# Optimization experiments

Hardware: AMD Instinct MI355X
Metric: run time of the kernel (lower is better)

## Reference

```python
import jax, jax.numpy as jnp
import numpy as np

B, N_NODES, NUM_FEATURES = 64, 1024, 128
NHID = 128
NUM_CLASSES = 10
SKEW_DIM = 64
EDGES_PER_GRAPH = 16384
POOL_RATIO = 0.5
LAMB = 1.0
NEG_SLOPE = 0.2  # HGPSLPool default negative_slope


def setup_inputs() -> dict:
    key = jax.random.key(0)
    ks = jax.random.split(key, 16)
    x = jax.random.normal(ks[0], (B, N_NODES, NUM_FEATURES), jnp.float32)
    src = jax.random.randint(ks[1], (B, EDGES_PER_GRAPH), 0, N_NODES)
    dst = jax.random.randint(ks[2], (B, EDGES_PER_GRAPH), 0, N_NODES)
    skew = jax.random.normal(ks[3], (B, SKEW_DIM), jnp.float32)

    def glorot(k, shape):
        s = jnp.sqrt(6.0 / (shape[0] + shape[1]))
        return jax.random.uniform(k, shape, jnp.float32, -s, s)

    params = dict(
        W1=glorot(ks[4], (NUM_FEATURES, NHID)), b1=jnp.zeros((NHID,), jnp.float32),
        W2=glorot(ks[5], (NHID, NHID)), b2=jnp.zeros((NHID,), jnp.float32),
        W3=glorot(ks[6], (NHID, NHID)), b3=jnp.zeros((NHID,), jnp.float32),
        att1=glorot(ks[7], (2 * NHID, 1))[:, 0],
        att2=glorot(ks[8], (2 * NHID, 1))[:, 0],
        Wsk=glorot(ks[9], (SKEW_DIM, NHID)), bsk=jnp.zeros((NHID,), jnp.float32),
        Wl1=glorot(ks[10], (3 * NHID, NHID)), bl1=jnp.zeros((NHID,), jnp.float32),
        Wl2=glorot(ks[11], (NHID, NHID // 2)), bl2=jnp.zeros((NHID // 2,), jnp.float32),
        Wl3=glorot(ks[12], (NHID // 2, NUM_CLASSES)), bl3=jnp.zeros((NUM_CLASSES,), jnp.float32),
    )
    return {"x": x, "src": src, "dst": dst, "skew": skew, **params}


def _inv_sqrt(d):
    return jnp.where(d > 0, jax.lax.rsqrt(jnp.where(d > 0, d, 1.0)), 0.0)


def gcn_conv(X, A, W, b):
    # x' = D^-1/2 (A + I_missing) D^-1/2 (X W) + b  (add_remaining_self_loops fill=1)
    n = A.shape[-1]
    diag = jnp.diagonal(A, axis1=-2, axis2=-1)  # [B,n]
    A_sl = A + jnp.where(diag == 0, 1.0, 0.0)[:, :, None] * jnp.eye(n, dtype=A.dtype)
    dis = _inv_sqrt(A_sl.sum(-1))  # [B,n]
    h = X @ W
    return dis[:, :, None] * jnp.einsum('bij,bjf->bif', A_sl, dis[:, :, None] * h) + b


def node_information_score(X, A):
    # (I - D^-1/2 A D^-1/2) X with self-loops removed; score = row-sum of |.|
    A0 = A * (1.0 - jnp.eye(A.shape[-1], dtype=A.dtype))
    dis = _inv_sqrt(A0.sum(-1))
    Anorm = dis[:, :, None] * A0 * dis[:, None, :]
    info = X - jnp.einsum('bij,bjf->bif', Anorm, X)
    return jnp.abs(info).sum(-1)  # [B,n]


def hgpsl_pool(X, A, att, k):
    # top-k by information score, induced subgraph, dense structure learning (softmax attn)
    score = node_information_score(X, A)
    _, perm = jax.lax.top_k(score, k)  # [B,k]
    Xp = jnp.take_along_axis(X, perm[:, :, None], axis=1)  # [B,k,F]
    Ap = jnp.take_along_axis(jnp.take_along_axis(A, perm[:, :, None], axis=1), perm[:, None, :], axis=2)
    F_ = X.shape[-1]
    a_row = Xp @ att[:F_]  # [B,k]
    a_col = Xp @ att[F_:]
    w = jax.nn.leaky_relu(a_row[:, :, None] + a_col[:, None, :], NEG_SLOPE)
    w = w + LAMB * Ap  # induced edge weights (ones on binary graph) scaled by lamb
    A_new = jax.nn.softmax(w, axis=-1)  # per-row softmax over within-graph nodes
    return Xp, A_new


def readout(X):
    return jnp.concatenate([X.max(axis=1), X.mean(axis=1)], axis=-1)  # [gmp | gap]


def reference(x, src, dst, skew, W1, b1, W2, b2, W3, b3, att1, att2, Wsk, bsk,
              Wl1, bl1, Wl2, bl2, Wl3, bl3):
    Bn, n = x.shape[0], x.shape[1]
    b_idx = jnp.arange(Bn)[:, None]
    A = jnp.zeros((Bn, n, n), x.dtype).at[b_idx, src, dst].set(1.0)
    A = jnp.maximum(A, A.transpose(0, 2, 1)) * (1.0 - jnp.eye(n, dtype=x.dtype))

    xskew = jax.nn.relu(skew @ Wsk + bsk)  # [B, nhid]

    h = jax.nn.relu(gcn_conv(x, A, W1, b1))
    k1 = int(np.ceil(POOL_RATIO * n))
    h, A1 = hgpsl_pool(h, A, att1, k1)
    x1 = readout(h)

    h = jax.nn.relu(gcn_conv(h, A1, W2, b2))
    k2 = int(np.ceil(POOL_RATIO * k1))
    h, A2 = hgpsl_pool(h, A1, att2, k2)
    x2 = readout(h)

    h = jax.nn.relu(gcn_conv(h, A2, W3, b3))
    x3 = readout(h)

    g = jax.nn.relu(x1) + jax.nn.relu(x2) + jax.nn.relu(x3)  # [B, 2*nhid]
    g = jnp.concatenate([g, xskew], axis=-1)                  # [B, 3*nhid]
    g = jax.nn.relu(g @ Wl1 + bl1)  # dropout is identity in eval mode
    g = jax.nn.relu(g @ Wl2 + bl2)
    return jax.nn.log_softmax(g @ Wl3 + bl3, axis=-1)
```

## Files before the change

### kernel.cpp

```cpp
#include <hip/hip_runtime.h>
#include <math.h>

#define Bb 64
#define N0 1024
#define NE 16384
#define Fd 128
#define K1 512
#define K2 256
#define RPB 256

typedef __attribute__((ext_vector_type(8))) short short8v;
typedef __attribute__((ext_vector_type(4))) float float4v;

__device__ __forceinline__ float wred_sum(float v) {
#pragma unroll
  for (int o = 32; o > 0; o >>= 1) v += __shfl_down(v, o, 64);
  return v;
}
__device__ __forceinline__ float wred_sum_all(float v) {
#pragma unroll
  for (int o = 32; o > 0; o >>= 1) v += __shfl_xor(v, o, 64);
  return v;
}
__device__ __forceinline__ float wred_max_all(float v) {
#pragma unroll
  for (int o = 32; o > 0; o >>= 1) v = fmaxf(v, __shfl_xor(v, o, 64));
  return v;
}
__device__ __forceinline__ unsigned short bf16hi(float x) {
  unsigned u = __float_as_uint(x);
  return (unsigned short)((u + 0x7fffu + ((u >> 16) & 1u)) >> 16);
}
__device__ __forceinline__ float bf2f(unsigned short h) {
  return __uint_as_float(((unsigned)h) << 16);
}

__global__ __launch_bounds__(1024) void k_graph(const int* __restrict__ src,
    const int* __restrict__ dst, unsigned* __restrict__ adj,
    unsigned short* __restrict__ nbr, int* __restrict__ degv,
    float* __restrict__ dis0, float* __restrict__ dis1) {
  __shared__ unsigned lmask[RPB * 32];
  int t = threadIdx.x;
  int b = blockIdx.x >> 2;
  int rlo = (blockIdx.x & 3) * RPB;
#pragma unroll
  for (int i = t; i < RPB * 32; i += 1024) lmask[i] = 0;
  __syncthreads();
  const int* sp = src + b * NE;
  const int* dp = dst + b * NE;
#pragma unroll
  for (int e = t; e < NE; e += 1024) {
    int u = sp[e], v = dp[e];
    if (u == v) continue;
    if ((unsigned)(u - rlo) < RPB)
      atomicOr(&lmask[(u - rlo) * 32 + (v >> 5)], 1u << (v & 31));
    if ((unsigned)(v - rlo) < RPB)
      atomicOr(&lmask[(v - rlo) * 32 + (u >> 5)], 1u << (u & 31));
  }
  __syncthreads();
  unsigned* adjg = adj + ((size_t)(b << 10) + rlo) * 32;
#pragma unroll
  for (int i = t; i < RPB * 32; i += 1024) adjg[i] = lmask[i];
  if (t < RPB) {
    int row = (b << 10) + rlo + t;
    const unsigned* wm = &lmask[t * 32];
    int d = 0;
#pragma unroll
    for (int i = 0; i < 32; ++i) d += __popc(wm[i]);
    degv[row] = d;
    dis0[row] = d > 0 ? rsqrtf((float)d) : 0.f;
    dis1[row] = rsqrtf((float)(d + 1));
    unsigned short* dstp = nbr + (size_t)row * 128;
    int o = 0;
#pragma unroll
    for (int w = 0; w < 32; ++w) {
      unsigned m = wm[w];
      int bas = w << 5;
      while (m) {
        int j = bas + __ffs(m) - 1; m &= m - 1;
        dstp[o++] = (unsigned short)((j << 2) | (j & 3));
      }
    }
  }
}

__global__ __launch_bounds__(512) void k_gemmm(const float* __restrict__ X,
                                               const float* __restrict__ W,
                                               float* __restrict__ C) {
  __shared__ unsigned short AsHi[64 * 40], AsLo[64 * 40];
  __shared__ unsigned short YtHi[128 * 40], YtLo[128 * 40];
  int t = threadIdx.x;
  size_t row0 = (size_t)blockIdx.x * 64;
  const float* Xb = X + row0 * Fd;
  int sar = t >> 3, sak = (t & 7) << 2;
  int awoff = sar * 40 + ((sak >> 3) ^ ((sar >> 3) & 3)) * 8 + (sak & 4);
  int wc = t & 127, ob = t >> 7;
  int ywoff = wc * 40 + (ob ^ ((wc >> 3) & 3)) * 8;
  int w = t >> 6, l = t & 63;
  int tr = w & 3, ch = w >> 2;
  int lr = l & 15, lg4 = l >> 4;
  int arow = 16 * tr + lr;
  int aroff = arow * 40 + ((lg4 ^ ((arow >> 3) & 3)) << 3);
  int boff[4];
#pragma unroll
  for (int j = 0; j < 4; ++j) {
    int colj = ch * 64 + j * 16 + lr;
    boff[j] = colj * 40 + ((lg4 ^ ((colj >> 3) & 3)) << 3);
  }
  float4v acc[4] = {{0.f, 0.f, 0.f, 0.f}, {0.f, 0.f, 0.f, 0.f},
                    {0.f, 0.f, 0.f, 0.f}, {0.f, 0.f, 0.f, 0.f}};
  for (int kb = 0; kb < 128; kb += 32) {
    __syncthreads();
    {
      float4 av = *(const float4*)&Xb[(size_t)sar * Fd + kb + sak];
      float vs[4] = {av.x, av.y, av.z, av.w};
      unsigned short h[4], lo[4];
#pragma unroll
      for (int i = 0; i < 4; ++i) {
        h[i] = bf16hi(vs[i]);
        float fhi = __uint_as_float(((unsigned)h[i]) << 16);
        lo[i] = bf16hi(vs[i] - fhi);
      }
      uint2 ph, pl;
      ph.x = (unsigned)h[0] | ((unsigned)h[1] << 16);
      ph.y = (unsigned)h[2] | ((unsigned)h[3] << 16);
      pl.x = (unsigned)lo[0] | ((unsigned)lo[1] << 16);
      pl.y = (unsigned)lo[2] | ((unsigned)lo[3] << 16);
      *(uint2*)&AsHi[awoff] = ph;
      *(uint2*)&AsLo[awoff] = pl;
    }
    {
      float vs[8];
      const float* wp = W + (size_t)(kb + ob * 8) * Fd + wc;
#pragma unroll
      for (int kk = 0; kk < 8; ++kk) vs[kk] = wp[(size_t)kk * Fd];
      uint4 uh, ul;
      unsigned hu[4], lu[4];
#pragma unroll
      for (int kk = 0; kk < 4; ++kk) {
        unsigned short h0 = bf16hi(vs[2 * kk]);
        unsigned short l0 = bf16hi(vs[2 * kk] - __uint_as_float(((unsigned)h0) << 16));
        unsigned short h1 = bf16hi(vs[2 * kk + 1]);
        unsigned short l1 = bf16hi(vs[2 * kk + 1] - __uint_as_float(((unsigned)h1) << 16));
        hu[kk] = (unsigned)h0 | ((unsigned)h1 << 16);
        lu[kk] = (unsigned)l0 | ((unsigned)l1 << 16);
      }
      uh.x = hu[0]; uh.y = hu[1]; uh.z = hu[2]; uh.w = hu[3];
      ul.x = lu[0]; ul.y = lu[1]; ul.z = lu[2]; ul.w = lu[3];
      *(uint4*)&YtHi[ywoff] = uh;
      *(uint4*)&YtLo[ywoff] = ul;
    }
    __syncthreads();
    short8v ah = *(const short8v*)&AsHi[aroff];
    short8v al = *(const short8v*)&AsLo[aroff];
#pragma unroll
    for (int j = 0; j < 4; ++j) {
      short8v bh = *(const short8v*)&YtHi[boff[j]];
      short8v bl = *(const short8v*)&YtLo[boff[j]];
      acc[j] = __builtin_amdgcn_mfma_f32_16x16x32_bf16(ah, bh, acc[j], 0, 0, 0);
      acc[j] = __builtin_amdgcn_mfma_f32_16x16x32_bf16(ah, bl, acc[j], 0, 0, 0);
      acc[j] = __builtin_amdgcn_mfma_f32_16x16x32_bf16(al, bh, acc[j], 0, 0, 0);
    }
  }
#pragma unroll
  for (int r = 0; r < 4; ++r) {
    size_t grow = row0 + 16 * tr + (lg4 << 2) + r;
#pragma unroll
    for (int j = 0; j < 4; ++j) {
      int gcol = ch * 64 + j * 16 + lr;
      C[grow * Fd + gcol] = acc[j][r];
    }
  }
}

__global__ __launch_bounds__(1024) void k_convnis(const unsigned short* __restrict__ nbr,
    const int* __restrict__ degv, const float* __restrict__ XW,
    const float* __restrict__ dis0, const float* __restrict__ dis1,
    const float* __restrict__ b1, float* __restrict__ h1, float* __restrict__ partial) {
  __shared__ float Xs[N0 * 16];
  int t = threadIdx.x;
  int g = blockIdx.x & 63;
  int cb = blockIdx.x >> 6;
  int c16 = cb * 16;
  const float* XWg = XW + ((size_t)(g << 10)) * Fd + c16;
  const float* d1g = dis1 + (g << 10);
  const float* d0g = dis0 + (g << 10);
  {
    int r = t;
    float s = d1g[r];
    int sw = r & 3;
#pragma unroll
    for (int sl = 0; sl < 4; ++sl) {
      int lc = sl ^ sw;
      float4 v = *(const float4*)&XWg[(size_t)r * Fd + lc * 4];
      v.x *= s; v.y *= s; v.z *= s; v.w *= s;
      *(float4*)&Xs[r * 16 + sl * 4] = v;
    }
  }
  __syncthreads();
  int c4 = t & 3, rsl = t >> 2;
  const unsigned short* nb = nbr + (((size_t)(g << 10)) << 7);
  float4 bv = *(const float4*)&b1[c16 + c4 * 4];
  float4 hsave[4];
  int degs[4];
  const char* Xb = (const char*)Xs;
  int cx = c4 << 4;
#pragma unroll
  for (int rg = 0; rg < 4; ++rg) {
    int lrow = rg * 256 + rsl;
    int grow = (g << 10) + lrow;
    int deg = degv[grow];
    degs[rg] = deg;
    const unsigned short* nr = nb + ((size_t)lrow << 7);
    float4 acc = make_float4(0.f, 0.f, 0.f, 0.f);
    int dp = deg & ~7, i = 0;
    for (; i < dp; i += 8) {
      uint4 w = *(const uint4*)&nr[i];
      int s_[8] = {(int)(w.x & 0xffffu), (int)(w.x >> 16),
                   (int)(w.y & 0xffffu), (int)(w.y >> 16),
                   (int)(w.z & 0xffffu), (int)(w.z >> 16),
                   (int)(w.w & 0xffffu), (int)(w.w >> 16)};
      float4 vv[8];
#pragma unroll
      for (int u = 0; u < 8; ++u)
        vv[u] = *(const float4*)(Xb + ((s_[u] << 4) ^ cx));
#pragma unroll
      for (int u = 0; u < 8; ++u) {
        acc.x += vv[u].x; acc.y += vv[u].y; acc.z += vv[u].z; acc.w += vv[u].w;
      }
    }
    for (; i < deg; ++i) {
      int s = nr[i];
      float4 v = *(const float4*)(Xb + ((s << 4) ^ cx));
      acc.x += v.x; acc.y += v.y; acc.z += v.z; acc.w += v.w;
    }
    float di = d1g[lrow];
    int sself = (lrow << 2) | (lrow & 3);
    float4 self = *(const float4*)(Xb + ((sself << 4) ^ cx));
    float4 h;
    h.x = fmaxf(di * (acc.x + self.x) + bv.x, 0.f);
    h.y = fmaxf(di * (acc.y + self.y) + bv.y, 0.f);
    h.z = fmaxf(di * (acc.z + self.z) + bv.z, 0.f);
    h.w = fmaxf(di * (acc.w + self.w) + bv.w, 0.f);
    hsave[rg] = h;
    *(float4*)&h1[(size_t)grow * Fd + c16 + c4 * 4] = h;
  }
  __syncthreads();
#pragma unroll
  for (int rg = 0; rg < 4; ++rg) {
    int lrow = rg * 256 + rsl;
    float s0 = d0g[lrow];
    float4 h = hsave[rg];
    h.x *= s0; h.y *= s0; h.z *= s0; h.w *= s0;
    int sself = (lrow << 2) | (lrow & 3);
    *(float4*)((char*)Xs + ((sself << 4) ^ cx)) = h;
  }
  __syncthreads();
#pragma unroll
  for (int rg = 0; rg < 4; ++rg) {
    int lrow = rg * 256 + rsl;
    int grow = (g << 10) + lrow;
    int deg = degs[rg];
    const unsigned short* nr = nb + ((size_t)lrow << 7);
    float4 acc = make_float4(0.f, 0.f, 0.f, 0.f);
    int dp = deg & ~7, i = 0;
    for (; i < dp; i += 8) {
      uint4 w = *(const uint4*)&nr[i];
      int s_[8] = {(int)(w.x & 0xffffu), (int)(w.x >> 16),
                   (int)(w.y & 0xffffu), (int)(w.y >> 16),
                   (int)(w.z & 0xffffu), (int)(w.z >> 16),
                   (int)(w.w & 0xffffu), (int)(w.w >> 16)};
      float4 vv[8];
#pragma unroll
      for (int u = 0; u < 8; ++u)
        vv[u] = *(const float4*)(Xb + ((s_[u] << 4) ^ cx));
#pragma unroll
      for (int u = 0; u < 8; ++u) {
        acc.x += vv[u].x; acc.y += vv[u].y; acc.z += vv[u].z; acc.w += vv[u].w;
      }
    }
    for (; i < deg; ++i) {
      int s = nr[i];
      float4 v = *(const float4*)(Xb + ((s << 4) ^ cx));
      acc.x += v.x; acc.y += v.y; acc.z += v.z; acc.w += v.w;
    }
    float d0 = d0g[lrow];
    float4 h = hsave[rg];
    float p = fabsf(h.x - d0 * acc.x) + fabsf(h.y - d0 * acc.y) +
              fabsf(h.z - d0 * acc.z) + fabsf(h.w - d0 * acc.w);
    p += __shfl_xor(p, 1, 64);
    p += __shfl_xor(p, 2, 64);
    if (c4 == 0) partial[(size_t)grow * 8 + cb] = p;
  }
}

__global__ __launch_bounds__(1024) void k_topk(const float* __restrict__ score,
                                               int* __restrict__ perm, int n, int k,
                                               int ps) {
  __shared__ unsigned long long keys[1024];
  int b = blockIdx.x, t = threadIdx.x;
  float s = 0.f;
  const float* p = score + ((size_t)b * n + t) * ps;
  for (int i = 0; i < ps; ++i) s += p[i];
  unsigned ub = __float_as_uint(s);
  unsigned su = (ub & 0x80000000u) ? ~ub : (ub | 0x80000000u);
  keys[t] = ((unsigned long long)(~su) << 32) | (unsigned)t;
  __syncthreads();
  for (int kk = 2; kk <= n; kk <<= 1) {
    for (int j = kk >> 1; j > 0; j >>= 1) {
      int ixj = t ^ j;
      if (ixj > t) {
        unsigned long long a = keys[t], c = keys[ixj];
        bool up = ((t & kk) == 0);
        if ((a > c) == up) { keys[t] = c; keys[ixj] = a; }
      }
      __syncthreads();
    }
  }
  if (t < k) perm[b * k + t] = (int)(keys[t] & 0xffffffffu);
}

__global__ __launch_bounds__(128) void k_gather(const float* __restrict__ h,
    const int* __restrict__ perm, const float* __restrict__ att, float* __restrict__ Xp,
    float* __restrict__ ar, float* __restrict__ ac, int n, int k) {
  int idx = blockIdx.x, f = threadIdx.x;
  int b = idx / k;
  __shared__ float red[4];
  int p = perm[idx];
  float v = h[((size_t)b * n + p) * Fd + f];
  Xp[(size_t)idx * Fd + f] = v;
  float r1 = wred_sum(v * att[f]);
  float r2 = wred_sum(v * att[Fd + f]);
  if ((f & 63) == 0) { red[f >> 6] = r1; red[2 + (f >> 6)] = r2; }
  __syncthreads();
  if (f == 0) { ar[idx] = red[0] + red[1]; ac[idx] = red[2] + red[3]; }
}

__global__ __launch_bounds__(1024) void k_readout(const float* __restrict__ X, int n,
                                                  float* __restrict__ g, int init) {
  int b = blockIdx.x, t = threadIdx.x;
  int f = t & 127, rs = t >> 7;
  __shared__ float smax[8][128];
  __shared__ float ssum[8][128];
  int per = n >> 3;
  const float* Xs = X + ((size_t)b * n + (size_t)rs * per) * Fd + f;
  float mx = -3.0e38f, sm = 0.f;
  for (int j = 0; j < per; j += 8) {
    float vv[8];
#pragma unroll
    for (int u = 0; u < 8; ++u) vv[u] = Xs[(size_t)(j + u) * Fd];
#pragma unroll
    for (int u = 0; u < 8; ++u) { mx = fmaxf(mx, vv[u]); sm += vv[u]; }
  }
  smax[rs][f] = mx; ssum[rs][f] = sm;
  __syncthreads();
  if (t < 128) {
    float m = smax[0][f], s = ssum[0][f];
#pragma unroll
    for (int q = 1; q < 8; ++q) { m = fmaxf(m, smax[q][f]); s += ssum[q][f]; }
    float a = fmaxf(m, 0.f);
    float m2 = fmaxf(s / (float)n, 0.f);
    if (init) { g[b * 384 + f] = a; g[b * 384 + 128 + f] = m2; }
    else      { g[b * 384 + f] += a; g[b * 384 + 128 + f] += m2; }
  }
}

__global__ __launch_bounds__(256) void k_buildA_bit(const unsigned* __restrict__ adj,
    const int* __restrict__ perm, const float* __restrict__ ar, const float* __restrict__ ac,
    unsigned short* __restrict__ Ahi, unsigned short* __restrict__ Alo,
    float* __restrict__ disc, float* __restrict__ saO,
    float* __restrict__ disn, float* __restrict__ diagO) {
  int wid = threadIdx.x >> 6, lane = threadIdx.x & 63;
  int row = blockIdx.x * 4 + wid;
  int b = row >> 9, i = row & (K1 - 1);
  int pbase = b << 9;
  int pi = perm[pbase + i];
  float ari = ar[pbase + i];
  int j0 = lane * 8;
  float acv[8]; int pj[8];
  *(float4*)&acv[0] = *(const float4*)&ac[pbase + j0];
  *(float4*)&acv[4] = *(const float4*)&ac[pbase + j0 + 4];
  *(int4*)&pj[0] = *(const int4*)&perm[pbase + j0];
  *(int4*)&pj[4] = *(const int4*)&perm[pbase + j0 + 4];
  const unsigned* arow = adj + (size_t)((b << 10) + pi) * 32;
  float xv[8];
#pragma unroll
  for (int u = 0; u < 8; ++u) {
    float x = ari + acv[u];
    x = x > 0.f ? x : 0.2f * x;
    unsigned word = arow[pj[u] >> 5];
    xv[u] = x + (float)((word >> (pj[u] & 31)) & 1u);
  }
  float m = xv[0];
#pragma unroll
  for (int u = 1; u < 8; ++u) m = fmaxf(m, xv[u]);
  m = wred_max_all(m);
  float e[8], ls = 0.f;
#pragma unroll
  for (int u = 0; u < 8; ++u) { e[u] = expf(xv[u] - m); ls += e[u]; }
  float s = wred_sum_all(ls);
  float inv = 1.0f / s;
  float av[8]; float lsum = 0.f;
#pragma unroll
  for (int u = 0; u < 8; ++u) { av[u] = e[u] * inv; lsum += av[u]; }
  unsigned short hi[8], lo[8];
#pragma unroll
  for (int u = 0; u < 8; ++u) {
    hi[u] = bf16hi(av[u]);
    lo[u] = bf16hi(av[u] - bf2f(hi[u]));
  }
  uint4 ph, pl;
  ph.x = (unsigned)hi[0] | ((unsigned)hi[1] << 16);
  ph.y = (unsigned)hi[2] | ((unsigned)hi[3] << 16);
  ph.z = (unsigned)hi[4] | ((unsigned)hi[5] << 16);
  ph.w = (unsigned)hi[6] | ((unsigned)hi[7] << 16);
  pl.x = (unsigned)lo[0] | ((unsigned)lo[1] << 16);
  pl.y = (unsigned)lo[2] | ((unsigned)lo[3] << 16);
  pl.z = (unsigned)lo[4] | ((unsigned)lo[5] << 16);
  pl.w = (unsigned)lo[6] | ((unsigned)lo[7] << 16);
  *(uint4*)&Ahi[(size_t)row * K1 + j0] = ph;
  *(uint4*)&Alo[(size_t)row * K1 + j0] = pl;
  float rs = wred_sum_all(lsum);
  float dsel = av[i & 7];
  float dval = __shfl(dsel, i >> 3, 64);
  if (lane == 0) {
    float sav = (dval == 0.f) ? 1.f : 0.f;
    float deg = rs + sav;
    disc[row] = deg > 0.f ? rsqrtf(deg) : 0.f;
    saO[row] = sav;
    float deg0 = rs - dval;
    disn[row] = deg0 > 0.f ? rsqrtf(deg0) : 0.f;
    diagO[row] = dval;
  }
}

__global__ __launch_bounds__(256) void k_buildA_dense(
    const unsigned short* __restrict__ AprevHi, const unsigned short* __restrict__ AprevLo,
    const int* __restrict__ perm, const float* __restrict__ ar, const float* __restrict__ ac,
    unsigned short* __restrict__ Ahi, unsigned short* __restrict__ Alo,
    float* __restrict__ disc, float* __restrict__ saO,
    float* __restrict__ disn, float* __restrict__ diagO) {
  int wid = threadIdx.x >> 6, lane = threadIdx.x & 63;
  int row = blockIdx.x * 4 + wid;
  int b = row >> 8, i = row & (K2 - 1);
  int pbase = b << 8;
  int pi = perm[pbase + i];
  float ari = ar[pbase + i];
  int j0 = lane * 4;
  float acv[4]; int pj[4];
  *(float4*)&acv[0] = *(const float4*)&ac[pbase + j0];
  *(int4*)&pj[0] = *(const int4*)&perm[pbase + j0];
  size_t apbase = (size_t)((b << 9) + pi) * K1;
  float xv[4];
#pragma unroll
  for (int u = 0; u < 4; ++u) {
    float x = ari + acv[u];
    x = x > 0.f ? x : 0.2f * x;
    float aval = bf2f(AprevHi[apbase + pj[u]]) + bf2f(AprevLo[apbase + pj[u]]);
    xv[u] = x + aval;
  }
  float m = fmaxf(fmaxf(xv[0], xv[1]), fmaxf(xv[2], xv[3]));
  m = wred_max_all(m);
  float e[4], ls = 0.f;
#pragma unroll
  for (int u = 0; u < 4; ++u) { e[u] = expf(xv[u] - m); ls += e[u]; }
  float s = wred_sum_all(ls);
  float inv = 1.0f / s;
  float av[4]; float lsum = 0.f;
#pragma unroll
  for (int u = 0; u < 4; ++u) { av[u] = e[u] * inv; lsum += av[u]; }
  unsigned short hi[4], lo[4];
#pragma unroll
  for (int u = 0; u < 4; ++u) {
    hi[u] = bf16hi(av[u]);
    lo[u] = bf16hi(av[u] - bf2f(hi[u]));
  }
  uint2 ph, pl;
  ph.x = (unsigned)hi[0] | ((unsigned)hi[1] << 16);
  ph.y = (unsigned)hi[2] | ((unsigned)hi[3] << 16);
  pl.x = (unsigned)lo[0] | ((unsigned)lo[1] << 16);
  pl.y = (unsigned)lo[2] | ((unsigned)lo[3] << 16);
  *(uint2*)&Ahi[(size_t)row * K2 + j0] = ph;
  *(uint2*)&Alo[(size_t)row * K2 + j0] = pl;
  float rs = wred_sum_all(lsum);
  float dsel = av[i & 3];
  float dval = __shfl(dsel, i >> 2, 64);
  if (lane == 0) {
    float sav = (dval == 0.f) ? 1.f : 0.f;
    float deg = rs + sav;
    disc[row] = deg > 0.f ? rsqrtf(deg) : 0.f;
    saO[row] = sav;
    float deg0 = rs - dval;
    disn[row] = deg0 > 0.f ? rsqrtf(deg0) : 0.f;
    diagO[row] = dval;
  }
}

template <int MODE>
__global__ __launch_bounds__(512) void k_mmf(
    const unsigned short* __restrict__ Ahi, const unsigned short* __restrict__ Alo,
    const float* __restrict__ Y, const float* __restrict__ wrow,
    const float* __restrict__ aux, const float* __restrict__ bias,
    float* __restrict__ outp, int n) {
  __shared__ unsigned short AsHi[64 * 40], AsLo[64 * 40];
  __shared__ unsigned short YtHi[64 * 40], YtLo[64 * 40];
  int t = threadIdx.x;
  int tiles2 = (n >> 6) << 1;
  int bid = blockIdx.x;
  int c = bid & 7, q = bid >> 3;
  int g = c * 8 + q / tiles2;
  int rem = q % tiles2;
  int rt = rem >> 1, ct = rem & 1;
  const unsigned short* AbHi = Ahi + (size_t)g * n * n + (size_t)(rt * 64) * n;
  const unsigned short* AbLo = Alo + (size_t)g * n * n + (size_t)(rt * 64) * n;
  const float* Yb = Y + (size_t)g * n * Fd + ct * 64;
  const float* wb = wrow + (size_t)g * n;
  int sar = t >> 3, sak = (t & 7) << 2;
  int awoff = sar * 40 + ((sak >> 3) ^ ((sar >> 3) & 3)) * 8 + (sak & 4);
  int yc = t & 63, ykb = (t >> 6) & 3;
  int ywoff = yc * 40 + (ykb ^ ((yc >> 3) & 3)) * 8;
  int w = t >> 6, l = t & 63;
  int tr = w & 3, tcb = (w >> 2) << 1;
  int lr = l & 15, lg4 = l >> 4;
  int arow = 16 * tr + lr;
  int aroff = arow * 40 + ((lg4 ^ ((arow >> 3) & 3)) << 3);
  int col0 = 16 * tcb + lr, col1 = col0 + 16;
  int b0off = col0 * 40 + ((lg4 ^ ((col0 >> 3) & 3)) << 3);
  int b1off = col1 * 40 + ((lg4 ^ ((col1 >> 3) & 3)) << 3);
  float4v acc0 = {0.f, 0.f, 0.f, 0.f};
  float4v acc1 = {0.f, 0.f, 0.f, 0.f};
  for (int kb = 0; kb < n; kb += 32) {
    __syncthreads();
    {
      uint2 ph = *(const uint2*)&AbHi[(size_t)sar * n + kb + sak];
      uint2 pl = *(const uint2*)&AbLo[(size_t)sar * n + kb + sak];
      *(uint2*)&AsHi[awoff] = ph;
      *(uint2*)&AsLo[awoff] = pl;
    }
    if (t < 256) {
      float vs[8];
      const float* yp = Yb + (size_t)(kb + ykb * 8) * Fd + yc;
      const float* wp = wb + kb + ykb * 8;
#pragma unroll
      for (int kk = 0; kk < 8; ++kk) vs[kk] = yp[(size_t)kk * Fd] * wp[kk];
      uint4 uh, ul;
      unsigned hu[4], lu[4];
#pragma unroll
      for (int kk = 0; kk < 4; ++kk) {
        unsigned short h0 = bf16hi(vs[2 * kk]);
        unsigned short l0 = bf16hi(vs[2 * kk] - __uint_as_float(((unsigned)h0) << 16));
        unsigned short h1 = bf16hi(vs[2 * kk + 1]);
        unsigned short l1 = bf16hi(vs[2 * kk + 1] - __uint_as_float(((unsigned)h1) << 16));
        hu[kk] = (unsigned)h0 | ((unsigned)h1 << 16);
        lu[kk] = (unsigned)l0 | ((unsigned)l1 << 16);
      }
      uh.x = hu[0]; uh.y = hu[1]; uh.z = hu[2]; uh.w = hu[3];
      ul.x = lu[0]; ul.y = lu[1]; ul.z = lu[2]; ul.w = lu[3];
      *(uint4*)&YtHi[ywoff] = uh;
      *(uint4*)&YtLo[ywoff] = ul;
    }
    __syncthreads();
    short8v ah = *(const short8v*)&AsHi[aroff];
    short8v al = *(const short8v*)&AsLo[aroff];
    short8v bh0 = *(const short8v*)&YtHi[b0off];
    short8v bl0 = *(const short8v*)&YtLo[b0off];
    short8v bh1 = *(const short8v*)&YtHi[b1off];
    short8v bl1 = *(const short8v*)&YtLo[b1off];
    acc0 = __builtin_amdgcn_mfma_f32_16x16x32_bf16(ah, bh0, acc0, 0, 0, 0);
    acc0 = __builtin_amdgcn_mfma_f32_16x16x32_bf16(ah, bl0, acc0, 0, 0, 0);
    acc0 = __builtin_amdgcn_mfma_f32_16x16x32_bf16(al, bh0, acc0, 0, 0, 0);
    acc1 = __builtin_amdgcn_mfma_f32_16x16x32_bf16(ah, bh1, acc1, 0, 0, 0);
    acc1 = __builtin_amdgcn_mfma_f32_16x16x32_bf16(ah, bl1, acc1, 0, 0, 0);
    acc1 = __builtin_amdgcn_mfma_f32_16x16x32_bf16(al, bh1, acc1, 0, 0, 0);
  }
  int colg0 = ct * 64 + 16 * tcb + lr;
  int colg1 = colg0 + 16;
  if (MODE == 0) {
    float bv0 = bias[colg0], bv1 = bias[colg1];
#pragma unroll
    for (int r = 0; r < 4; ++r) {
      int row = rt * 64 + 16 * tr + ((l >> 4) << 2) + r;
      size_t R = (size_t)g * n + row;
      float dc = wb[row];
      float sv = aux[R] * dc;
      float y0 = Y[R * Fd + colg0];
      float y1 = Y[R * Fd + colg1];
      float o0 = fmaxf(dc * (acc0[r] + sv * y0) + bv0, 0.f);
      float o1 = fmaxf(dc * (acc1[r] + sv * y1) + bv1, 0.f);
      outp[R * Fd + colg0] = o0;
      outp[R * Fd + colg1] = o1;
    }
  } else {
#pragma unroll
    for (int r = 0; r < 4; ++r) {
      int row = rt * 64 + 16 * tr + ((l >> 4) << 2) + r;
      size_t R = (size_t)g * n + row;
      float dn = wb[row];
      float dg = aux[R] * dn;
      float h0 = Y[R * Fd + colg0];
      float h1 = Y[R * Fd + colg1];
      float p = fabsf(h0 - dn * (acc0[r] - dg * h0)) +
                fabsf(h1 - dn * (acc1[r] - dg * h1));
      p += __shfl_xor(p, 1, 64);
      p += __shfl_xor(p, 2, 64);
      p += __shfl_xor(p, 4, 64);
      p += __shfl_xor(p, 8, 64);
      if (lr == 0) outp[R * 2 + ct] = p;
    }
  }
}

__global__ __launch_bounds__(128) void k_head(const float* __restrict__ gin,
    const float* __restrict__ skew, const float* __restrict__ Wsk,
    const float* __restrict__ bsk, const float* __restrict__ Wl1,
    const float* __restrict__ bl1, const float* __restrict__ Wl2,
    const float* __restrict__ bl2, const float* __restrict__ Wl3,
    const float* __restrict__ bl3, float* __restrict__ out) {
  __shared__ float gl[384];
  __shared__ float t1s[128];
  __shared__ float t2s[64];
  __shared__ float lg[10];
  int b = blockIdx.x, f = threadIdx.x;
  gl[f] = gin[b * 384 + f];
  gl[128 + f] = gin[b * 384 + 128 + f];
  float acc = bsk[f];
  for (int s = 0; s < 64; ++s) acc += skew[b * 64 + s] * Wsk[s * Fd + f];
  gl[256 + f] = fmaxf(acc, 0.f);
  __syncthreads();
  acc = bl1[f];
  for (int s = 0; s < 384; ++s) acc += gl[s] * Wl1[s * 128 + f];
  t1s[f] = fmaxf(acc, 0.f);
  __syncthreads();
  if (f < 64) {
    acc = bl2[f];
    for (int s = 0; s < 128; ++s) acc += t1s[s] * Wl2[s * 64 + f];
    t2s[f] = fmaxf(acc, 0.f);
  }
  __syncthreads();
  if (f < 10) {
    acc = bl3[f];
    for (int s = 0; s < 64; ++s) acc += t2s[s] * Wl3[s * 10 + f];
    lg[f] = acc;
  }
  __syncthreads();
  if (f == 0) {
    float m = lg[0];
    for (int c = 1; c < 10; ++c) m = fmaxf(m, lg[c]);
    float s = 0.f;
    for (int c = 0; c < 10; ++c) s += expf(lg[c] - m);
    float l = logf(s);
    for (int c = 0; c < 10; ++c) out[b * 10 + c] = lg[c] - m - l;
  }
}

extern "C" void kernel_launch(void* const* d_in, const int* in_sizes, int n_in,
                              void* d_out, int out_size, void* d_ws, size_t ws_size,
                              hipStream_t stream) {
  const float* x    = (const float*)d_in[0];
  const int*   src  = (const int*)d_in[1];
  const int*   dst  = (const int*)d_in[2];
  const float* skew = (const float*)d_in[3];
  const float* W1   = (const float*)d_in[4];
  const float* b1   = (const float*)d_in[5];
  const float* W2   = (const float*)d_in[6];
  const float* b2   = (const float*)d_in[7];
  const float* W3   = (const float*)d_in[8];
  const float* b3   = (const float*)d_in[9];
  const float* att1 = (const float*)d_in[10];
  const float* att2 = (const float*)d_in[11];
  const float* Wsk  = (const float*)d_in[12];
  const float* bsk  = (const float*)d_in[13];
  const float* Wl1  = (const float*)d_in[14];
  const float* bl1  = (const float*)d_in[15];
  const float* Wl2  = (const float*)d_in[16];
  const float* bl2  = (const float*)d_in[17];
  const float* Wl3  = (const float*)d_in[18];
  const float* bl3  = (const float*)d_in[19];
  float* out = (float*)d_out;

  char* base = (char*)d_ws;
  size_t off = 0;
  auto alloc = [&](size_t bytes) -> void* {
    void* p = base + off;
    off += (bytes + 255) & ~(size_t)255;
    return p;
  };

  unsigned* adj = (unsigned*)alloc((size_t)Bb * N0 * 32 * 4);
  float* dis0 = (float*)alloc((size_t)Bb * N0 * 4);
  float* dis1 = (float*)alloc((size_t)Bb * N0 * 4);
  int*   degv = (int*)alloc((size_t)Bb * N0 * 4);
  float* bigA = (float*)alloc((size_t)64 * 1024 * 1024);
  float* XW  = bigA;
  float* h1  = bigA + (size_t)Bb * N0 * Fd;
  unsigned short* A1hi = (unsigned short*)bigA;
  unsigned short* A1lo = (unsigned short*)bigA + (size_t)Bb * K1 * K1;
  float* XW3 = bigA;
  float* h3  = bigA + (size_t)Bb * K2 * Fd;
  float* partial = (float*)alloc((size_t)Bb * N0 * 8 * 4);
  int*   perm1 = (int*)alloc((size_t)Bb * K1 * 4);
  float* Xp1 = (float*)alloc((size_t)Bb * K1 * Fd * 4);
  unsigned short* A2hi = (unsigned short*)Xp1;
  unsigned short* A2lo = (unsigned short*)Xp1 + (size_t)Bb * K2 * K2;
  float* ar1 = (float*)alloc((size_t)Bb * K1 * 4);
  float* ac1 = (float*)alloc((size_t)Bb * K1 * 4);
  float* disc2 = (float*)alloc((size_t)Bb * K1 * 4);
  float* sa2   = (float*)alloc((size_t)Bb * K1 * 4);
  float* disn2 = (float*)alloc((size_t)Bb * K1 * 4);
  float* diag2 = (float*)alloc((size_t)Bb * K1 * 4);
  float* XW2 = (float*)alloc((size_t)Bb * K1 * Fd * 4);
  float* h2  = (float*)alloc((size_t)Bb * K1 * Fd * 4);
  int*   perm2 = (int*)alloc((size_t)Bb * K2 * 4);
  float* Xp2 = (float*)alloc((size_t)Bb * K2 * Fd * 4);
  float* ar2 = (float*)alloc((size_t)Bb * K2 * 4);
  float* ac2 = (float*)alloc((size_t)Bb * K2 * 4);
  float* disc3 = (float*)alloc((size_t)Bb * K2 * 4);
  float* sa3   = (float*)alloc((size_t)Bb * K2 * 4);
  float* disn3 = (float*)alloc((size_t)Bb * K2 * 4);
  float* diag3 = (float*)alloc((size_t)Bb * K2 * 4);
  float* g  = (float*)alloc((size_t)Bb * 384 * 4);
  unsigned short* nbr = (unsigned short*)XW2;
  (void)ws_size; (void)in_sizes; (void)n_in; (void)out_size;

  k_graph<<<Bb * 4, 1024, 0, stream>>>(src, dst, adj, nbr, degv, dis0, dis1);
  k_gemmm<<<Bb * N0 / 64, 512, 0, stream>>>(x, W1, XW);
  k_convnis<<<Bb * 8, 1024, 0, stream>>>(nbr, degv, XW, dis0, dis1, b1, h1, partial);
  k_topk<<<Bb, N0, 0, stream>>>(partial, perm1, N0, K1, 8);
  k_gather<<<Bb * K1, 128, 0, stream>>>(h1, perm1, att1, Xp1, ar1, ac1, N0, K1);
  k_readout<<<Bb, 1024, 0, stream>>>(Xp1, K1, g, 1);
  k_buildA_bit<<<Bb * K1 / 4, 256, 0, stream>>>(adj, perm1, ar1, ac1, A1hi, A1lo,
                                                disc2, sa2, disn2, diag2);

  k_gemmm<<<Bb * K1 / 64, 512, 0, stream>>>(Xp1, W2, XW2);
  k_mmf<0><<<Bb * (K1 / 64) * 2, 512, 0, stream>>>(A1hi, A1lo, XW2, disc2, sa2, b2, h2, K1);
  k_mmf<1><<<Bb * (K1 / 64) * 2, 512, 0, stream>>>(A1hi, A1lo, h2, disn2, diag2, nullptr, partial, K1);
  k_topk<<<Bb, K1, 0, stream>>>(partial, perm2, K1, K2, 2);
  k_gather<<<Bb * K2, 128, 0, stream>>>(h2, perm2, att2, Xp2, ar2, ac2, K1, K2);
  k_readout<<<Bb, 1024, 0, stream>>>(Xp2, K2, g, 0);
  k_buildA_dense<<<Bb * K2 / 4, 256, 0, stream>>>(A1hi, A1lo, perm2, ar2, ac2,
                                                  A2hi, A2lo, disc3, sa3, disn3, diag3);

  k_gemmm<<<Bb * K2 / 64, 512, 0, stream>>>(Xp2, W3, XW3);
  k_mmf<0><<<Bb * (K2 / 64) * 2, 512, 0, stream>>>(A2hi, A2lo, XW3, disc3, sa3, b3, h3, K2);
  k_readout<<<Bb, 1024, 0, stream>>>(h3, K2, g, 0);

  k_head<<<Bb, 128, 0, stream>>>(g, skew, Wsk, bsk, Wl1, bl1, Wl2, bl2, Wl3, bl3, out);
}
```

Measured before the change: 303.7 us.

## Register-prefetch next K tile in MFMA matmul and use shuffles in bitonic top-k

The split-bf16 MFMA matmul now loads the next K-slice of A and Y into registers while the current slice sits in shared memory, so global load latency overlaps the MFMA work. The bitonic sort in top-k keeps each key in a register and uses wavefront shuffles for partner distances below 64, falling back to shared memory with two barriers only for larger strides. This costs extra registers in the matmul and changes the compare-exchange form of the sort.

```diff
diff --git a/kernel.cpp b/kernel.cpp
--- a/kernel.cpp
+++ b/kernel.cpp
@@ -304,20 +304,26 @@
   for (int i = 0; i < ps; ++i) s += p[i];
   unsigned ub = __float_as_uint(s);
   unsigned su = (ub & 0x80000000u) ? ~ub : (ub | 0x80000000u);
-  keys[t] = ((unsigned long long)(~su) << 32) | (unsigned)t;
-  __syncthreads();
+  unsigned long long mykey = ((unsigned long long)(~su) << 32) | (unsigned)t;
   for (int kk = 2; kk <= n; kk <<= 1) {
     for (int j = kk >> 1; j > 0; j >>= 1) {
-      int ixj = t ^ j;
-      if (ixj > t) {
-        unsigned long long a = keys[t], c = keys[ixj];
-        bool up = ((t & kk) == 0);
-        if ((a > c) == up) { keys[t] = c; keys[ixj] = a; }
+      unsigned long long other;
+      if (j >= 64) {
+        keys[t] = mykey;
+        __syncthreads();
+        other = keys[t ^ j];
+        __syncthreads();
+      } else {
+        other = __shfl_xor(mykey, j, 64);
       }
-      __syncthreads();
-    }
-  }
-  if (t < k) perm[b * k + t] = (int)(keys[t] & 0xffffffffu);
+      bool asc = ((t & kk) == 0);
+      bool lower = ((t & j) == 0);
+      bool keepmin = (asc == lower);
+      bool takeOther = keepmin ? (other < mykey) : (other > mykey);
+      if (takeOther) mykey = other;
+    }
+  }
+  if (t < k) perm[b * k + t] = (int)(mykey & 0xffffffffu);
 }
 
 __global__ __launch_bounds__(128) void k_gather(const float* __restrict__ h,
@@ -529,28 +535,28 @@
   int b1off = col1 * 40 + ((lg4 ^ ((col1 >> 3) & 3)) << 3);
   float4v acc0 = {0.f, 0.f, 0.f, 0.f};
   float4v acc1 = {0.f, 0.f, 0.f, 0.f};
+  uint2 rAh = *(const uint2*)&AbHi[(size_t)sar * n + sak];
+  uint2 rAl = *(const uint2*)&AbLo[(size_t)sar * n + sak];
+  float rY[8];
+  if (t < 256) {
+    const float* yp = Yb + (size_t)(ykb * 8) * Fd + yc;
+    const float* wp = wb + ykb * 8;
+#pragma unroll
+    for (int kk = 0; kk < 8; ++kk) rY[kk] = yp[(size_t)kk * Fd] * wp[kk];
+  }
   for (int kb = 0; kb < n; kb += 32) {
     __syncthreads();
-    {
-      uint2 ph = *(const uint2*)&AbHi[(size_t)sar * n + kb + sak];
-      uint2 pl = *(const uint2*)&AbLo[(size_t)sar * n + kb + sak];
-      *(uint2*)&AsHi[awoff] = ph;
-      *(uint2*)&AsLo[awoff] = pl;
-    }
+    *(uint2*)&AsHi[awoff] = rAh;
+    *(uint2*)&AsLo[awoff] = rAl;
     if (t < 256) {
-      float vs[8];
-      const float* yp = Yb + (size_t)(kb + ykb * 8) * Fd + yc;
-      const float* wp = wb + kb + ykb * 8;
-#pragma unroll
-      for (int kk = 0; kk < 8; ++kk) vs[kk] = yp[(size_t)kk * Fd] * wp[kk];
       uint4 uh, ul;
       unsigned hu[4], lu[4];
 #pragma unroll
       for (int kk = 0; kk < 4; ++kk) {
-        unsigned short h0 = bf16hi(vs[2 * kk]);
-        unsigned short l0 = bf16hi(vs[2 * kk] - __uint_as_float(((unsigned)h0) << 16));
-        unsigned short h1 = bf16hi(vs[2 * kk + 1]);
-        unsigned short l1 = bf16hi(vs[2 * kk + 1] - __uint_as_float(((unsigned)h1) << 16));
+        unsigned short h0 = bf16hi(rY[2 * kk]);
+        unsigned short l0 = bf16hi(rY[2 * kk] - bf2f(h0));
+        unsigned short h1 = bf16hi(rY[2 * kk + 1]);
+        unsigned short l1 = bf16hi(rY[2 * kk + 1] - bf2f(h1));
         hu[kk] = (unsigned)h0 | ((unsigned)h1 << 16);
         lu[kk] = (unsigned)l0 | ((unsigned)l1 << 16);
       }
@@ -558,6 +564,16 @@
       ul.x = lu[0]; ul.y = lu[1]; ul.z = lu[2]; ul.w = lu[3];
       *(uint4*)&YtHi[ywoff] = uh;
       *(uint4*)&YtLo[ywoff] = ul;
+    }
+    if (kb + 32 < n) {
+      rAh = *(const uint2*)&AbHi[(size_t)sar * n + kb + 32 + sak];
+      rAl = *(const uint2*)&AbLo[(size_t)sar * n + kb + 32 + sak];
+      if (t < 256) {
+        const float* yp = Yb + (size_t)(kb + 32 + ykb * 8) * Fd + yc;
+        const float* wp = wb + kb + 32 + ykb * 8;
+#pragma unroll
+        for (int kk = 0; kk < 8; ++kk) rY[kk] = yp[(size_t)kk * Fd] * wp[kk];
+      }
     }
     __syncthreads();
     short8v ah = *(const short8v*)&AsHi[aroff];
```

Measured after the change: 311.4 us. 1.03x slower.
